# Optimization experiments

Hardware: AMD Instinct MI355X
Metric: run time of the kernel (lower is better)

## Reference

```python
import jax, jax.numpy as jnp
import numpy as np

B, T, I, H, O = 512, 512, 128, 512, 128


def setup_inputs() -> dict:
    key = jax.random.key(0)
    k = jax.random.split(key, 6)
    si = 1.0 / np.sqrt(I)
    sh = 1.0 / np.sqrt(H)
    x = jax.random.normal(k[0], (B, T, I), dtype=jnp.float32)
    # gate order along last axis: [g, i, f, o] (each H wide)
    Wx = jax.random.uniform(k[1], (I, 4 * H), jnp.float32, -si, si)
    Wh = jax.random.uniform(k[2], (H, 4 * H), jnp.float32, -sh, sh)
    b = jax.random.uniform(k[3], (4 * H,), jnp.float32, -sh, sh)
    Wp = jax.random.uniform(k[4], (H, O), jnp.float32, -sh, sh)
    bp = jax.random.uniform(k[5], (O,), jnp.float32, -sh, sh)
    return {"x": x, "Wx": Wx, "Wh": Wh, "b": b, "Wp": Wp, "bp": bp}


def reference(x, Wx, Wh, b, Wp, bp):
    # x: [B, T, I]. Fused LSTM: one input GEMM + one hidden GEMM per step,
    # gates split from the concatenated [g, i, f, o] projection.
    Bsz = x.shape[0]
    Hd = Wh.shape[0]
    # Precompute all input projections in one big GEMM: [T, B, 4H]
    xz = jnp.einsum('bti,ij->tbj', x, Wx)

    def step(carry, xzt):
        h, c = carry
        z = xzt + h @ Wh + b  # [B, 4H]
        g, i, f, o = jnp.split(z, 4, axis=-1)
        g = jnp.tanh(g)
        i = jax.nn.sigmoid(i)
        f = jax.nn.sigmoid(f)
        o = jax.nn.sigmoid(o)
        c = g * i + c * f
        h = jnp.tanh(c) * o
        return (h, c), None

    h0 = jnp.zeros((Bsz, Hd), dtype=x.dtype)
    c0 = jnp.zeros((Bsz, Hd), dtype=x.dtype)
    (h, c), _ = jax.lax.scan(step, (h0, c0), xz)
    p = h @ Wp + bp  # [B, O]
    return jax.nn.softmax(p, axis=1)
```

## Files before the change

### kernel.cpp

```cpp
#include <hip/hip_runtime.h>
#include <hip/hip_cooperative_groups.h>

namespace cg = cooperative_groups;

typedef _Float16 f16;
typedef _Float16 half8 __attribute__((ext_vector_type(8)));
typedef float float4v __attribute__((ext_vector_type(4)));
typedef int int4v __attribute__((ext_vector_type(4)));

constexpr int kB  = 512;
constexpr int kT  = 512;
constexpr int kI  = 128;
constexpr int kH  = 512;
constexpr int kNG = 2048;
constexpr int kO  = 128;

constexpr int LDK = 650;

__device__ __forceinline__ float fsig(float v)  { return 1.0f / (1.0f + __expf(-v)); }
__device__ __forceinline__ float ftanh(float v) { return 1.0f - 2.0f / (1.0f + __expf(2.0f * v)); }

union h8u { half8 h; int4v i; };
union f16u { f16 f; unsigned short s; };

__global__ __launch_bounds__(256, 1) void lstm_fused(
    const float* __restrict__ x,  const float* __restrict__ Wx,
    const float* __restrict__ Wh, const float* __restrict__ bias,
    const float* __restrict__ Wp, const float* __restrict__ bp,
    float* __restrict__ out, float* __restrict__ ws)
{
  cg::grid_group grid = cg::this_grid();

  __shared__ __align__(16) f16 w_lds[64 * LDK];

  const int tid = threadIdx.x;
  const int wg  = blockIdx.x;
  const int bg  = wg & 7;
  const int ng  = wg >> 3;
  const int b0  = bg * 64;
  const int wv  = tid >> 6;
  const int l   = tid & 63;
  const int lc  = l & 15;
  const int lj  = l >> 4;

  f16* h16a = (f16*)ws;
  f16* h16b = h16a + kB * kH;
  unsigned* flags = (unsigned*)(h16b + kB * kH);

  {
    int gtid = wg * 256 + tid;
    unsigned* p = (unsigned*)h16a;
    p[gtid * 2] = 0u; p[gtid * 2 + 1] = 0u;
    if (gtid < 32768) flags[gtid] = 0u;
  }

  for (int idx = tid; idx < 64 * 640; idx += 256) {
    int c = idx & 63;
    int k = idx >> 6;
    int gcol = (c >> 4) * 512 + ng * 16 + (c & 15);
    float v = (k < 512) ? Wh[(long)k * kNG + gcol]
                        : Wx[(long)(k - 512) * kNG + gcol];
    w_lds[c * LDK + k] = (f16)v;
  }
  float bb[4];
  #pragma unroll
  for (int g = 0; g < 4; ++g) bb[g] = bias[g * 512 + ng * 16 + lc];

  float ce[4] = {0.f, 0.f, 0.f, 0.f};
  const int arow = b0 + wv * 16 + lc;
  const f16* wbase = w_lds + lc * LDK + lj * 8;
  const float* xrow = x + (long)arow * (kT * kI) + lj * 8;

  float4v xa[4], xb[4];
  #pragma unroll
  for (int q = 0; q < 4; ++q) {
    xa[q] = *(const float4v*)(xrow + q * 32);
    xb[q] = *(const float4v*)(xrow + q * 32 + 4);
  }

  grid.sync();

  unsigned* myslot = flags + (((unsigned)(bg * 32 + ng) * 4u + (unsigned)wv) * 32u);
  const unsigned* poll0 = flags + (((unsigned)(bg * 32 + (l & 31)) * 4u + (unsigned)(l >> 5)) * 32u);
  const unsigned* poll1 = flags + (((unsigned)(bg * 32 + (l & 31)) * 4u + (unsigned)((l >> 5) + 2)) * 32u);

  float4v xacc[4];
  #pragma unroll
  for (int g = 0; g < 4; ++g) xacc[g] = float4v{bb[g], bb[g], bb[g], bb[g]};
  #pragma unroll
  for (int q = 0; q < 4; ++q) {
    half8 a;
    #pragma unroll
    for (int e = 0; e < 4; ++e) { a[e] = (f16)xa[q][e]; a[e + 4] = (f16)xb[q][e]; }
    #pragma unroll
    for (int g = 0; g < 4; ++g) {
      half8 bf = *(const half8*)(wbase + g * 16 * LDK + 512 + q * 32);
      xacc[g] = __builtin_amdgcn_mfma_f32_16x16x32_f16(a, bf, xacc[g], 0, 0, 0);
    }
  }
  #pragma unroll
  for (int q = 0; q < 4; ++q) {
    xa[q] = *(const float4v*)(xrow + kI + q * 32);
    xb[q] = *(const float4v*)(xrow + kI + q * 32 + 4);
  }

  const unsigned hoff = (unsigned)(arow * kH * 2 + lj * 16);

  for (int t = 0; t < kT; ++t) {
    const f16* hc = (t & 1) ? h16b : h16a;
    f16*       hn = (t & 1) ? h16a : h16b;

    h8u ah[16];
    #pragma unroll
    for (int p = 0; p < 16; ++p) {
      asm volatile("global_load_dwordx4 %0, %1, %2 offset:%c3 sc0 sc1"
                   : "=v"(ah[p].i)
                   : "v"(hoff), "s"(hc), "i"(p * 64));
    }
    asm volatile("s_waitcnt vmcnt(0)" ::: "memory");
    __builtin_amdgcn_sched_barrier(0);

    float4v acc[4];
    #pragma unroll
    for (int g = 0; g < 4; ++g) acc[g] = xacc[g];
    #pragma unroll
    for (int ks = 0; ks < 16; ++ks) {
      #pragma unroll
      for (int g = 0; g < 4; ++g) {
        half8 bf = *(const half8*)(wbase + g * 16 * LDK + ks * 32);
        acc[g] = __builtin_amdgcn_mfma_f32_16x16x32_f16(ah[ks].h, bf, acc[g], 0, 0, 0);
      }
    }

    #pragma unroll
    for (int e = 0; e < 4; ++e) {
      float gv = ftanh(acc[0][e]);
      float iv = fsig(acc[1][e]);
      float fv = fsig(acc[2][e]);
      float ov = fsig(acc[3][e]);
      float cn = gv * iv + ce[e] * fv;
      ce[e] = cn;
      f16u u; u.f = (f16)(ftanh(cn) * ov);
      unsigned short* dst = (unsigned short*)hn
          + (long)(b0 + wv * 16 + lj * 4 + e) * kH + ng * 16 + lc;
      __hip_atomic_store(dst, u.s, __ATOMIC_RELAXED, __HIP_MEMORY_SCOPE_AGENT);
    }

    asm volatile("s_waitcnt vmcnt(0)" ::: "memory");
    if (l == 0)
      __hip_atomic_store(myslot, (unsigned)(t + 1), __ATOMIC_RELAXED, __HIP_MEMORY_SCOPE_AGENT);

    if (t + 1 < kT) {
      #pragma unroll
      for (int g = 0; g < 4; ++g) xacc[g] = float4v{bb[g], bb[g], bb[g], bb[g]};
      #pragma unroll
      for (int q = 0; q < 4; ++q) {
        half8 a;
        #pragma unroll
        for (int e = 0; e < 4; ++e) { a[e] = (f16)xa[q][e]; a[e + 4] = (f16)xb[q][e]; }
        #pragma unroll
        for (int g = 0; g < 4; ++g) {
          half8 bf = *(const half8*)(wbase + g * 16 * LDK + 512 + q * 32);
          xacc[g] = __builtin_amdgcn_mfma_f32_16x16x32_f16(a, bf, xacc[g], 0, 0, 0);
        }
      }
      if (t + 2 < kT) {
        const float* xn = xrow + (long)(t + 2) * kI;
        #pragma unroll
        for (int q = 0; q < 4; ++q) {
          xa[q] = *(const float4v*)(xn + q * 32);
          xb[q] = *(const float4v*)(xn + q * 32 + 4);
        }
      }
    }

    {
      const unsigned tgt = (unsigned)(t + 1);
      unsigned v0, v1;
      do {
        v0 = __hip_atomic_load(poll0, __ATOMIC_RELAXED, __HIP_MEMORY_SCOPE_AGENT);
        v1 = __hip_atomic_load(poll1, __ATOMIC_RELAXED, __HIP_MEMORY_SCOPE_AGENT);
        v0 = (v0 < v1) ? v0 : v1;
      } while (__all((int)(v0 >= tgt)) == 0);
    }
  }

  grid.sync();

  const f16* hf = h16a;
  float* hrow = (float*)w_lds;
  float* red  = (float*)w_lds + 2 * kH;
  for (int i = tid; i < 2 * kH; i += 256) {
    int r = i >> 9, k = i & 511;
    hrow[i] = (float)hf[(long)(wg * 2 + r) * kH + k];
  }
  __syncthreads();

  const int orow = tid >> 7;
  const int oc   = tid & 127;
  float p = bp[oc];
  #pragma unroll 8
  for (int k = 0; k < kH; ++k)
    p += hrow[orow * kH + k] * Wp[(long)k * kO + oc];

  red[tid] = p;
  __syncthreads();
  float m = -1e30f;
  for (int j = 0; j < 128; ++j) m = fmaxf(m, red[orow * 128 + j]);
  __syncthreads();
  float e = __expf(p - m);
  red[tid] = e;
  __syncthreads();
  float s = 0.f;
  for (int j = 0; j < 128; ++j) s += red[orow * 128 + j];
  out[(long)(wg * 2 + orow) * kO + oc] = e / s;
}

extern "C" void kernel_launch(void* const* d_in, const int* in_sizes, int n_in,
                              void* d_out, int out_size, void* d_ws, size_t ws_size,
                              hipStream_t stream) {
  const float* x  = (const float*)d_in[0];
  const float* Wx = (const float*)d_in[1];
  const float* Wh = (const float*)d_in[2];
  const float* b  = (const float*)d_in[3];
  const float* Wp = (const float*)d_in[4];
  const float* bp = (const float*)d_in[5];
  float* out = (float*)d_out;
  float* ws  = (float*)d_ws;

  void* args[] = { &x, &Wx, &Wh, &b, &Wp, &bp, &out, &ws };
  hipLaunchCooperativeKernel((void*)lstm_fused, dim3(256), dim3(256), args, 0, stream);
}
```

Before: 6.125 ms.

## Halve grid and interleave two independent batch groups per workgroup to hide sync latency

The kernel now launches 128 workgroups instead of 256. Each workgroup owns two batch groups (p and p+4) for the same 16-column gate slice and alternates between them within each timestep. While one batch group waits on its peers' flags, the other group's GEMM and gate math can proceed, which is meant to hide the cross-workgroup spin-wait latency. Flags move to one per workgroup per batch group, set after a __syncthreads rather than per wave. The trade-off is more serial work per workgroup and use of only half the compute units.

```diff
diff --git a/kernel.cpp b/kernel.cpp
--- a/kernel.cpp
+++ b/kernel.cpp
@@ -35,23 +35,26 @@
 
   const int tid = threadIdx.x;
   const int wg  = blockIdx.x;
-  const int bg  = wg & 7;
-  const int ng  = wg >> 3;
-  const int b0  = bg * 64;
+  const int p   = wg >> 5;
+  const int ng  = wg & 31;
   const int wv  = tid >> 6;
   const int l   = tid & 63;
   const int lc  = l & 15;
   const int lj  = l >> 4;
 
+  const int bgp = p;
+  const int bgq = p + 4;
+
   f16* h16a = (f16*)ws;
   f16* h16b = h16a + kB * kH;
   unsigned* flags = (unsigned*)(h16b + kB * kH);
 
   {
     int gtid = wg * 256 + tid;
-    unsigned* p = (unsigned*)h16a;
-    p[gtid * 2] = 0u; p[gtid * 2 + 1] = 0u;
-    if (gtid < 32768) flags[gtid] = 0u;
+    unsigned* z = (unsigned*)h16a;
+    z[gtid * 4 + 0] = 0u; z[gtid * 4 + 1] = 0u;
+    z[gtid * 4 + 2] = 0u; z[gtid * 4 + 3] = 0u;
+    if (gtid < 8192) flags[gtid] = 0u;
   }
 
   for (int idx = tid; idx < 64 * 640; idx += 256) {
@@ -66,93 +69,127 @@
   #pragma unroll
   for (int g = 0; g < 4; ++g) bb[g] = bias[g * 512 + ng * 16 + lc];
 
-  float ce[4] = {0.f, 0.f, 0.f, 0.f};
-  const int arow = b0 + wv * 16 + lc;
   const f16* wbase = w_lds + lc * LDK + lj * 8;
-  const float* xrow = x + (long)arow * (kT * kI) + lj * 8;
-
-  float4v xa[4], xb[4];
-  #pragma unroll
-  for (int q = 0; q < 4; ++q) {
-    xa[q] = *(const float4v*)(xrow + q * 32);
-    xb[q] = *(const float4v*)(xrow + q * 32 + 4);
-  }
+
+  const int arow_p = bgp * 64 + wv * 16 + lc;
+  const int arow_q = bgq * 64 + wv * 16 + lc;
+  const float* xrow_p = x + (long)arow_p * (kT * kI) + lj * 8;
+  const float* xrow_q = x + (long)arow_q * (kT * kI) + lj * 8;
+  const unsigned hoff_p = (unsigned)(arow_p * kH * 2 + lj * 16);
+  const unsigned hoff_q = (unsigned)(arow_q * kH * 2 + lj * 16);
+
+  unsigned* slot_p = flags + (unsigned)(bgp * 32 + ng) * 32u;
+  unsigned* slot_q = flags + (unsigned)(bgq * 32 + ng) * 32u;
+  const unsigned* poll_p = flags + (unsigned)(bgp * 32 + (l & 31)) * 32u;
+  const unsigned* poll_q = flags + (unsigned)(bgq * 32 + (l & 31)) * 32u;
+
+  float ce_p[4] = {0.f, 0.f, 0.f, 0.f};
+  float ce_q[4] = {0.f, 0.f, 0.f, 0.f};
 
   grid.sync();
 
-  unsigned* myslot = flags + (((unsigned)(bg * 32 + ng) * 4u + (unsigned)wv) * 32u);
-  const unsigned* poll0 = flags + (((unsigned)(bg * 32 + (l & 31)) * 4u + (unsigned)(l >> 5)) * 32u);
-  const unsigned* poll1 = flags + (((unsigned)(bg * 32 + (l & 31)) * 4u + (unsigned)((l >> 5) + 2)) * 32u);
-
-  float4v xacc[4];
-  #pragma unroll
-  for (int g = 0; g < 4; ++g) xacc[g] = float4v{bb[g], bb[g], bb[g], bb[g]};
-  #pragma unroll
-  for (int q = 0; q < 4; ++q) {
-    half8 a;
-    #pragma unroll
-    for (int e = 0; e < 4; ++e) { a[e] = (f16)xa[q][e]; a[e + 4] = (f16)xb[q][e]; }
-    #pragma unroll
-    for (int g = 0; g < 4; ++g) {
-      half8 bf = *(const half8*)(wbase + g * 16 * LDK + 512 + q * 32);
-      xacc[g] = __builtin_amdgcn_mfma_f32_16x16x32_f16(a, bf, xacc[g], 0, 0, 0);
-    }
-  }
-  #pragma unroll
-  for (int q = 0; q < 4; ++q) {
-    xa[q] = *(const float4v*)(xrow + kI + q * 32);
-    xb[q] = *(const float4v*)(xrow + kI + q * 32 + 4);
-  }
-
-  const unsigned hoff = (unsigned)(arow * kH * 2 + lj * 16);
+  float4v xacc_p[4], xacc_q[4];
+  {
+    float4v xa[4], xb[4];
+    #pragma unroll
+    for (int q = 0; q < 4; ++q) {
+      xa[q] = *(const float4v*)(xrow_p + q * 32);
+      xb[q] = *(const float4v*)(xrow_p + q * 32 + 4);
+    }
+    #pragma unroll
+    for (int g = 0; g < 4; ++g) xacc_p[g] = float4v{bb[g], bb[g], bb[g], bb[g]};
+    #pragma unroll
+    for (int q = 0; q < 4; ++q) {
+      half8 a;
+      #pragma unroll
+      for (int e = 0; e < 4; ++e) { a[e] = (f16)xa[q][e]; a[e + 4] = (f16)xb[q][e]; }
+      #pragma unroll
+      for (int g = 0; g < 4; ++g) {
+        half8 bf = *(const half8*)(wbase + g * 16 * LDK + 512 + q * 32);
+        xacc_p[g] = __builtin_amdgcn_mfma_f32_16x16x32_f16(a, bf, xacc_p[g], 0, 0, 0);
+      }
+    }
+    #pragma unroll
+    for (int q = 0; q < 4; ++q) {
+      xa[q] = *(const float4v*)(xrow_q + q * 32);
+      xb[q] = *(const float4v*)(xrow_q + q * 32 + 4);
+    }
+    #pragma unroll
+    for (int g = 0; g < 4; ++g) xacc_q[g] = float4v{bb[g], bb[g], bb[g], bb[g]};
+    #pragma unroll
+    for (int q = 0; q < 4; ++q) {
+      half8 a;
+      #pragma unroll
+      for (int e = 0; e < 4; ++e) { a[e] = (f16)xa[q][e]; a[e + 4] = (f16)xb[q][e]; }
+      #pragma unroll
+      for (int g = 0; g < 4; ++g) {
+        half8 bf = *(const half8*)(wbase + g * 16 * LDK + 512 + q * 32);
+        xacc_q[g] = __builtin_amdgcn_mfma_f32_16x16x32_f16(a, bf, xacc_q[g], 0, 0, 0);
+      }
+    }
+  }
 
   for (int t = 0; t < kT; ++t) {
     const f16* hc = (t & 1) ? h16b : h16a;
     f16*       hn = (t & 1) ? h16a : h16b;
-
-    h8u ah[16];
-    #pragma unroll
-    for (int p = 0; p < 16; ++p) {
-      asm volatile("global_load_dwordx4 %0, %1, %2 offset:%c3 sc0 sc1"
-                   : "=v"(ah[p].i)
-                   : "v"(hoff), "s"(hc), "i"(p * 64));
-    }
-    asm volatile("s_waitcnt vmcnt(0)" ::: "memory");
-    __builtin_amdgcn_sched_barrier(0);
-
-    float4v acc[4];
-    #pragma unroll
-    for (int g = 0; g < 4; ++g) acc[g] = xacc[g];
-    #pragma unroll
-    for (int ks = 0; ks < 16; ++ks) {
-      #pragma unroll
-      for (int g = 0; g < 4; ++g) {
-        half8 bf = *(const half8*)(wbase + g * 16 * LDK + ks * 32);
-        acc[g] = __builtin_amdgcn_mfma_f32_16x16x32_f16(ah[ks].h, bf, acc[g], 0, 0, 0);
-      }
-    }
-
-    #pragma unroll
-    for (int e = 0; e < 4; ++e) {
-      float gv = ftanh(acc[0][e]);
-      float iv = fsig(acc[1][e]);
-      float fv = fsig(acc[2][e]);
-      float ov = fsig(acc[3][e]);
-      float cn = gv * iv + ce[e] * fv;
-      ce[e] = cn;
-      f16u u; u.f = (f16)(ftanh(cn) * ov);
-      unsigned short* dst = (unsigned short*)hn
-          + (long)(b0 + wv * 16 + lj * 4 + e) * kH + ng * 16 + lc;
-      __hip_atomic_store(dst, u.s, __ATOMIC_RELAXED, __HIP_MEMORY_SCOPE_AGENT);
-    }
-
-    asm volatile("s_waitcnt vmcnt(0)" ::: "memory");
-    if (l == 0)
-      __hip_atomic_store(myslot, (unsigned)(t + 1), __ATOMIC_RELAXED, __HIP_MEMORY_SCOPE_AGENT);
-
-    if (t + 1 < kT) {
-      #pragma unroll
-      for (int g = 0; g < 4; ++g) xacc[g] = float4v{bb[g], bb[g], bb[g], bb[g]};
+    const int  tx1 = (t + 1 < kT) ? (t + 1) : t;
+    const unsigned tgt = (unsigned)t;
+
+    {
+      unsigned v;
+      do {
+        v = __hip_atomic_load(poll_p, __ATOMIC_RELAXED, __HIP_MEMORY_SCOPE_AGENT);
+      } while (__all((int)(v >= tgt)) == 0);
+
+      float4v xa[4], xb[4];
+      const float* xn = xrow_p + (long)tx1 * kI;
+      #pragma unroll
+      for (int q = 0; q < 4; ++q) {
+        xa[q] = *(const float4v*)(xn + q * 32);
+        xb[q] = *(const float4v*)(xn + q * 32 + 4);
+      }
+      h8u ah[16];
+      #pragma unroll
+      for (int f = 0; f < 16; ++f) {
+        asm volatile("global_load_dwordx4 %0, %1, %2 offset:%c3 sc0 sc1"
+                     : "=v"(ah[f].i)
+                     : "v"(hoff_p), "s"(hc), "i"(f * 64));
+      }
+      asm volatile("s_waitcnt vmcnt(0)" ::: "memory");
+      __builtin_amdgcn_sched_barrier(0);
+
+      float4v acc[4];
+      #pragma unroll
+      for (int g = 0; g < 4; ++g) acc[g] = xacc_p[g];
+      #pragma unroll
+      for (int ks = 0; ks < 16; ++ks) {
+        #pragma unroll
+        for (int g = 0; g < 4; ++g) {
+          half8 bf = *(const half8*)(wbase + g * 16 * LDK + ks * 32);
+          acc[g] = __builtin_amdgcn_mfma_f32_16x16x32_f16(ah[ks].h, bf, acc[g], 0, 0, 0);
+        }
+      }
+
+      #pragma unroll
+      for (int e = 0; e < 4; ++e) {
+        float gv = ftanh(acc[0][e]);
+        float iv = fsig(acc[1][e]);
+        float fv = fsig(acc[2][e]);
+        float ov = fsig(acc[3][e]);
+        float cn = gv * iv + ce_p[e] * fv;
+        ce_p[e] = cn;
+        f16u u; u.f = (f16)(ftanh(cn) * ov);
+        unsigned short* dst = (unsigned short*)hn
+            + (long)(bgp * 64 + wv * 16 + lj * 4 + e) * kH + ng * 16 + lc;
+        __hip_atomic_store(dst, u.s, __ATOMIC_RELAXED, __HIP_MEMORY_SCOPE_AGENT);
+      }
+
+      __syncthreads();
+      if (tid == 0)
+        __hip_atomic_store(slot_p, (unsigned)(t + 1), __ATOMIC_RELAXED, __HIP_MEMORY_SCOPE_AGENT);
+
+      #pragma unroll
+      for (int g = 0; g < 4; ++g) xacc_p[g] = float4v{bb[g], bb[g], bb[g], bb[g]};
       #pragma unroll
       for (int q = 0; q < 4; ++q) {
         half8 a;
@@ -161,27 +198,77 @@
         #pragma unroll
         for (int g = 0; g < 4; ++g) {
           half8 bf = *(const half8*)(wbase + g * 16 * LDK + 512 + q * 32);
-          xacc[g] = __builtin_amdgcn_mfma_f32_16x16x32_f16(a, bf, xacc[g], 0, 0, 0);
+          xacc_p[g] = __builtin_amdgcn_mfma_f32_16x16x32_f16(a, bf, xacc_p[g], 0, 0, 0);
         }
       }
-      if (t + 2 < kT) {
-        const float* xn = xrow + (long)(t + 2) * kI;
-        #pragma unroll
-        for (int q = 0; q < 4; ++q) {
-          xa[q] = *(const float4v*)(xn + q * 32);
-          xb[q] = *(const float4v*)(xn + q * 32 + 4);
+    }
+
+    {
+      unsigned v;
+      do {
+        v = __hip_atomic_load(poll_q, __ATOMIC_RELAXED, __HIP_MEMORY_SCOPE_AGENT);
+      } while (__all((int)(v >= tgt)) == 0);
+
+      float4v xa[4], xb[4];
+      const float* xn = xrow_q + (long)tx1 * kI;
+      #pragma unroll
+      for (int q = 0; q < 4; ++q) {
+        xa[q] = *(const float4v*)(xn + q * 32);
+        xb[q] = *(const float4v*)(xn + q * 32 + 4);
+      }
+      h8u ah[16];
+      #pragma unroll
+      for (int f = 0; f < 16; ++f) {
+        asm volatile("global_load_dwordx4 %0, %1, %2 offset:%c3 sc0 sc1"
+                     : "=v"(ah[f].i)
+                     : "v"(hoff_q), "s"(hc), "i"(f * 64));
+      }
+      asm volatile("s_waitcnt vmcnt(0)" ::: "memory");
+      __builtin_amdgcn_sched_barrier(0);
+
+      float4v acc[4];
+      #pragma unroll
+      for (int g = 0; g < 4; ++g) acc[g] = xacc_q[g];
+      #pragma unroll
+      for (int ks = 0; ks < 16; ++ks) {
+        #pragma unroll
+        for (int g = 0; g < 4; ++g) {
+          half8 bf = *(const half8*)(wbase + g * 16 * LDK + ks * 32);
+          acc[g] = __builtin_amdgcn_mfma_f32_16x16x32_f16(ah[ks].h, bf, acc[g], 0, 0, 0);
         }
       }
-    }
-
-    {
-      const unsigned tgt = (unsigned)(t + 1);
-      unsigned v0, v1;
-      do {
-        v0 = __hip_atomic_load(poll0, __ATOMIC_RELAXED, __HIP_MEMORY_SCOPE_AGENT);
-        v1 = __hip_atomic_load(poll1, __ATOMIC_RELAXED, __HIP_MEMORY_SCOPE_AGENT);
-        v0 = (v0 < v1) ? v0 : v1;
-      } while (__all((int)(v0 >= tgt)) == 0);
+
+      #pragma unroll
+      for (int e = 0; e < 4; ++e) {
+        float gv = ftanh(acc[0][e]);
+        float iv = fsig(acc[1][e]);
+        float fv = fsig(acc[2][e]);
+        float ov = fsig(acc[3][e]);
+        float cn = gv * iv + ce_q[e] * fv;
+        ce_q[e] = cn;
+        f16u u; u.f = (f16)(ftanh(cn) * ov);
+        unsigned short* dst = (unsigned short*)hn
+            + (long)(bgq * 64 + wv * 16 + lj * 4 + e) * kH + ng * 16 + lc;
+        __hip_atomic_store(dst, u.s, __ATOMIC_RELAXED, __HIP_MEMORY_SCOPE_AGENT);
+      }
+
+      __syncthreads();
+      if (tid == 0)
+        __hip_atomic_store(slot_q, (unsigned)(t + 1), __ATOMIC_RELAXED, __HIP_MEMORY_SCOPE_AGENT);
+
+      #pragma unroll
+      for (int g = 0; g < 4; ++g) xacc_q[g] = float4v{bb[g], bb[g], bb[g], bb[g]};
+      #pragma unroll
+      for (int q = 0; q < 4; ++q) {
+        half8 a;
+        #pragma unroll
+        for (int e = 0; e < 4; ++e) { a[e] = (f16)xa[q][e]; a[e + 4] = (f16)xb[q][e]; }
+        #pragma unroll
+        for (int g = 0; g < 4; ++g) {
+          half8 bf = *(const half8*)(wbase + g * 16 * LDK + 512 + q * 32);
+          xacc_q[g] = __builtin_amdgcn_mfma_f32_16x16x32_f16(a, bf, xacc_q[g], 0, 0, 0);
+        }
+      }
     }
   }
 
@@ -190,30 +277,35 @@
   const f16* hf = h16a;
   float* hrow = (float*)w_lds;
   float* red  = (float*)w_lds + 2 * kH;
-  for (int i = tid; i < 2 * kH; i += 256) {
-    int r = i >> 9, k = i & 511;
-    hrow[i] = (float)hf[(long)(wg * 2 + r) * kH + k];
-  }
-  __syncthreads();
-
   const int orow = tid >> 7;
   const int oc   = tid & 127;
-  float p = bp[oc];
-  #pragma unroll 8
-  for (int k = 0; k < kH; ++k)
-    p += hrow[orow * kH + k] * Wp[(long)k * kO + oc];
-
-  red[tid] = p;
-  __syncthreads();
-  float m = -1e30f;
-  for (int j = 0; j < 128; ++j) m = fmaxf(m, red[orow * 128 + j]);
-  __syncthreads();
-  float e = __expf(p - m);
-  red[tid] = e;
-  __syncthreads();
-  float s = 0.f;
-  for (int j = 0; j < 128; ++j) s += red[orow * 128 + j];
-  out[(long)(wg * 2 + orow) * kO + oc] = e / s;
+
+  for (int pass = 0; pass < 2; ++pass) {
+    const int rbase = wg * 4 + pass * 2;
+    __syncthreads();
+    for (int i = tid; i < 2 * kH; i += 256) {
+      int r = i >> 9, k = i & 511;
+      hrow[i] = (float)hf[(long)(rbase + r) * kH + k];
+    }
+    __syncthreads();
+
+    float pv = bp[oc];
+    #pragma unroll 8
+    for (int k = 0; k < kH; ++k)
+      pv += hrow[orow * kH + k] * Wp[(long)k * kO + oc];
+
+    red[tid] = pv;
+    __syncthreads();
+    float m = -1e30f;
+    for (int j = 0; j < 128; ++j) m = fmaxf(m, red[orow * 128 + j]);
+    __syncthreads();
+    float e = __expf(pv - m);
+    red[tid] = e;
+    __syncthreads();
+    float s = 0.f;
+    for (int j = 0; j < 128; ++j) s += red[orow * 128 + j];
+    out[(long)(rbase + orow) * kO + oc] = e / s;
+  }
 }
 
 extern "C" void kernel_launch(void* const* d_in, const int* in_sizes, int n_in,
@@ -229,5 +321,5 @@
   float* ws  = (float*)d_ws;
 
   void* args[] = { &x, &Wx, &Wh, &b, &Wp, &bp, &out, &ws };
-  hipLaunchCooperativeKernel((void*)lstm_fused, dim3(256), dim3(256), args, 0, stream);
+  hipLaunchCooperativeKernel((void*)lstm_fused, dim3(128), dim3(256), args, 0, stream);
 }
```

Result: slower. 10.85 ms (+77.2%).
